# Kernel tuning notes

Measured on AMD Instinct MI355X. Metric: run time of the kernel, lower is better.

Reference implementation:

```python
import jax, jax.numpy as jnp
import numpy as np

D_MODEL = 1024
NUM_HEADS = 16
HEAD_DIM = D_MODEL // NUM_HEADS


def setup_inputs() -> dict:
    key = jax.random.key(0)
    ks = jax.random.split(key, 11)
    B, S, D = 2, 2048, D_MODEL
    scale = 1.0 / np.sqrt(D)
    inp = {
        "query": jax.random.normal(ks[0], (B, S, D), jnp.float32),
        "key": jax.random.normal(ks[1], (B, S, D), jnp.float32),
        "value": jax.random.normal(ks[2], (B, S, D), jnp.float32),
        "Wq": jax.random.normal(ks[3], (D, D), jnp.float32) * scale,
        "bq": jnp.zeros((D,), jnp.float32),
        "Wk": jax.random.normal(ks[4], (D, D), jnp.float32) * scale,
        "bk": jnp.zeros((D,), jnp.float32),
        "Wv": jax.random.normal(ks[5], (D, D), jnp.float32) * scale,
        "bv": jnp.zeros((D,), jnp.float32),
        "Wo": jax.random.normal(ks[6], (D, D), jnp.float32) * scale,
        "bo": jnp.zeros((D,), jnp.float32),
    }
    return inp


def reference(query, key, value, Wq, bq, Wk, bk, Wv, bv, Wo, bo):
    B, S, D = query.shape
    H, hd = NUM_HEADS, HEAD_DIM
    # linear projections (x @ W^T + b, torch nn.Linear convention)
    Q = query @ Wq.T + bq
    K = key @ Wk.T + bk
    V = value @ Wv.T + bv
    # split heads: [B, S, H, hd] -> [B, H, S, hd]
    Q = Q.reshape(B, S, H, hd).transpose(0, 2, 1, 3)
    K = K.reshape(B, S, H, hd).transpose(0, 2, 1, 3)
    V = V.reshape(B, S, H, hd).transpose(0, 2, 1, 3)
    # scaled dot-product attention (explicit, non-flash)
    scores = jnp.einsum("bhqd,bhkd->bhqk", Q, K) / jnp.sqrt(jnp.float32(hd)).astype(Q.dtype)
    attn = jax.nn.softmax(scores, axis=-1)
    out = jnp.einsum("bhqk,bhkd->bhqd", attn, V)
    # merge heads: [B, H, S, hd] -> [B, S, D]
    out = out.transpose(0, 2, 1, 3).reshape(B, S, D)
    return out @ Wo.T + bo
```

## Files before the change

### kernel.cpp

```cpp
#include <hip/hip_runtime.h>
#include <hip/hip_bf16.h>


constexpr int D_MODEL = 1024;
constexpr int S_LEN   = 2048;
constexpr int BATCH   = 2;
constexpr int NH      = 16;
constexpr int HD      = 64;
constexpr int ROWS    = BATCH * S_LEN;

typedef __attribute__((ext_vector_type(8))) short short8;
typedef __attribute__((ext_vector_type(4))) float float4a;

static __device__ __forceinline__ unsigned short f2bf(float f) {
  union { float f; unsigned u; } v{f};
  unsigned r = v.u + 0x7FFFu + ((v.u >> 16) & 1u);
  return (unsigned short)(r >> 16);
}

static __device__ __forceinline__ void async16(const void* g, void* l) {
  __builtin_amdgcn_global_load_lds(
      (const __attribute__((address_space(1))) unsigned int*)g,
      (__attribute__((address_space(3))) unsigned int*)l, 16, 0, 0);
}

struct ConvArgs { const float* s[7]; unsigned short* d[7]; int n[7]; };

__global__ __launch_bounds__(256) void convert_bf16(ConvArgs a) {
  const int which = blockIdx.y;
  const int i = (blockIdx.x * 256 + threadIdx.x) * 8;
  if (i >= a.n[which]) return;
  const float4* s = (const float4*)(a.s[which] + i);
  float4 x = s[0], y = s[1];
  unsigned short t[8] = {f2bf(x.x), f2bf(x.y), f2bf(x.z), f2bf(x.w),
                         f2bf(y.x), f2bf(y.y), f2bf(y.z), f2bf(y.w)};
  *(short8*)(a.d[which] + i) = *(short8*)t;
}

template <int MODE>
static __device__ __forceinline__ void gemm_body(const unsigned short* __restrict__ A,
                                                 const unsigned short* __restrict__ W,
                                                 const float* __restrict__ bias,
                                                 void* __restrict__ Yv, float scale) {
  __shared__ unsigned short As[128][32];
  __shared__ unsigned short Bs[128][32];
  const int tid = threadIdx.x;
  const int w = tid >> 6, lane = tid & 63;
  const int l15 = lane & 15, quad = lane >> 4;
  const int row0 = blockIdx.x * 128, col0 = blockIdx.y * 128;
  const int wm = (w & 1) * 64, wn = (w >> 1) * 64;

  const int srow = (w * 128 + lane) >> 2;
  const int schk = lane & 3;
  const unsigned short* Ap = A + (size_t)(row0 + srow) * D_MODEL + schk * 8;
  const unsigned short* Wp = W + (size_t)(col0 + srow) * D_MODEL + schk * 8;
  char* lA0 = (char*)As + w * 2048;
  char* lA1 = lA0 + 1024;
  char* lB0 = (char*)Bs + w * 2048;
  char* lB1 = lB0 + 1024;

  float4a acc[4][4];
#pragma unroll
  for (int i = 0; i < 4; i++)
#pragma unroll
    for (int j = 0; j < 4; j++) acc[i][j] = (float4a){0.f, 0.f, 0.f, 0.f};

  for (int kt = 0; kt < D_MODEL; kt += 32) {
    __syncthreads();
    async16(Ap + kt, lA0);
    async16(Ap + kt + 16 * D_MODEL, lA1);
    async16(Wp + kt, lB0);
    async16(Wp + kt + 16 * D_MODEL, lB1);
    __syncthreads();

    short8 af[4], bf[4];
#pragma unroll
    for (int mt = 0; mt < 4; mt++)
      af[mt] = *(const short8*)&As[wm + mt * 16 + l15][quad * 8];
#pragma unroll
    for (int nt = 0; nt < 4; nt++)
      bf[nt] = *(const short8*)&Bs[wn + nt * 16 + l15][quad * 8];
#pragma unroll
    for (int mt = 0; mt < 4; mt++)
#pragma unroll
      for (int nt = 0; nt < 4; nt++)
        acc[mt][nt] = __builtin_amdgcn_mfma_f32_16x16x32_bf16(af[mt], bf[nt], acc[mt][nt], 0, 0, 0);
  }

  int cols[4];
  float bvs[4];
#pragma unroll
  for (int nt = 0; nt < 4; nt++) {
    cols[nt] = col0 + wn + nt * 16 + l15;
    bvs[nt]  = bias[cols[nt]] * ((MODE == 0) ? scale : 1.0f);
  }

  if constexpr (MODE == 0) {
    unsigned short* Y = (unsigned short*)Yv;
#pragma unroll
    for (int mt = 0; mt < 4; mt++)
#pragma unroll
      for (int r = 0; r < 4; r++) {
        const int m = row0 + wm + mt * 16 + quad * 4 + r;
        const int bb = m >> 11, s = m & 2047;
#pragma unroll
        for (int nt = 0; nt < 4; nt++) {
          const int h = cols[nt] >> 6, d = cols[nt] & 63;
          Y[(((size_t)(bb * NH + h)) * S_LEN + s) * HD + d] =
              f2bf(acc[mt][nt][r] * scale + bvs[nt]);
        }
      }
  } else if constexpr (MODE == 2) {
    __shared__ unsigned short T[4][64][64];
#pragma unroll
    for (int mt = 0; mt < 4; mt++)
#pragma unroll
      for (int r = 0; r < 4; r++) {
        const int sl = mt * 16 + quad * 4 + r;
        const int cch = sl >> 3;
#pragma unroll
        for (int nt = 0; nt < 4; nt++) {
          const int dl = nt * 16 + l15;
          const int slot = cch ^ (dl & 7);
          T[w][dl][slot * 8 + (sl & 7)] = f2bf(acc[mt][nt][r] + bvs[nt]);
        }
      }
    asm volatile("s_waitcnt lgkmcnt(0)" ::: "memory");
    unsigned short* Y = (unsigned short*)Yv;
#pragma unroll
    for (int j = 0; j < 8; j++) {
      const int cid = j * 64 + lane;
      const int dl = cid >> 3;
      const int c  = cid & 7;
      const int slot = c ^ (dl & 7);
      short8 v = *(const short8*)&T[w][dl][slot * 8];
      const int col = col0 + wn + dl;
      const int h = col >> 6, d = col & 63;
      const int m = row0 + wm + c * 8;
      const int bb = m >> 11, s = m & 2047;
      *(short8*)&Y[(((size_t)(bb * NH + h)) * HD + d) * S_LEN + s] = v;
    }
  } else {
    float* Y = (float*)Yv;
#pragma unroll
    for (int mt = 0; mt < 4; mt++)
#pragma unroll
      for (int r = 0; r < 4; r++) {
        const int m = row0 + wm + mt * 16 + quad * 4 + r;
#pragma unroll
        for (int nt = 0; nt < 4; nt++)
          Y[(size_t)m * D_MODEL + cols[nt]] = acc[mt][nt][r] + bvs[nt];
      }
  }
}

__global__ __launch_bounds__(256) void gemm_qk(const unsigned short* q16, const unsigned short* k16,
                                               const unsigned short* wq, const unsigned short* wk,
                                               const float* bq, const float* bk,
                                               unsigned short* Q, unsigned short* K) {
  const bool z = (blockIdx.z != 0);
  gemm_body<0>(z ? k16 : q16, z ? wk : wq, z ? bk : bq, z ? (void*)K : (void*)Q,
               z ? 1.0f : 0.125f);
}

__global__ __launch_bounds__(256) void gemm_v(const unsigned short* v16, const unsigned short* wv,
                                              const float* bv, unsigned short* Vt) {
  gemm_body<2>(v16, wv, bv, Vt, 1.0f);
}

__global__ __launch_bounds__(256) void gemm_o(const unsigned short* o16, const unsigned short* wo,
                                              const float* bo, float* out) {
  gemm_body<3>(o16, wo, bo, out, 1.0f);
}

__global__ __launch_bounds__(256) void attn_kernel(
    const unsigned short* __restrict__ Qh, const unsigned short* __restrict__ Kh,
    const unsigned short* __restrict__ Vt, unsigned short* __restrict__ O) {
  const int qb = blockIdx.x;
  const int h  = blockIdx.y;
  const int bb = blockIdx.z;
  const int tid = threadIdx.x;
  const int w = tid >> 6, lane = tid & 63;
  const int l15 = lane & 15, quad = lane >> 4;

  __shared__ unsigned short Ks[64][72];
  __shared__ unsigned short Vs[64][72];
  __shared__ unsigned short Ps[4][32][72];

  const size_t bh = (size_t)(bb * NH + h);
  const unsigned short* Qp = Qh + bh * S_LEN * HD;
  const unsigned short* Kp = Kh + bh * S_LEN * HD;
  const unsigned short* Vp = Vt + bh * (size_t)HD * S_LEN;

  short8 qf[2][2];
#pragma unroll
  for (int qnt = 0; qnt < 2; qnt++)
#pragma unroll
    for (int c = 0; c < 2; c++)
      qf[qnt][c] = *(const short8*)(Qp + (size_t)(qb * 128 + w * 32 + qnt * 16 + l15) * HD +
                                    c * 32 + quad * 8);

  float4a Oacc[2][4];
#pragma unroll
  for (int a = 0; a < 2; a++)
#pragma unroll
    for (int b = 0; b < 4; b++) Oacc[a][b] = (float4a){0.f, 0.f, 0.f, 0.f};
  float lp[2] = {0.f, 0.f};

  for (int kb = 0; kb < S_LEN; kb += 64) {
    __syncthreads();
    {
      const unsigned short* src = Kp + (size_t)kb * HD;
#pragma unroll
      for (int r = 0; r < 2; r++) {
        const int idx = tid + r * 256;
        const int row = idx >> 3, cb = (idx & 7) * 8;
        *(short8*)&Ks[row][cb] = *(const short8*)(src + row * HD + cb);
      }
      const unsigned short* vsrc = Vp + kb;
#pragma unroll
      for (int r = 0; r < 2; r++) {
        const int idx = tid + r * 256;
        const int row = idx >> 3, cb = (idx & 7) * 8;
        *(short8*)&Vs[row][cb] = *(const short8*)(vsrc + (size_t)row * S_LEN + cb);
      }
    }
    __syncthreads();

#pragma unroll
    for (int mt = 0; mt < 4; mt++) {
      short8 a0 = *(const short8*)&Ks[mt * 16 + l15][quad * 8];
      short8 a1 = *(const short8*)&Ks[mt * 16 + l15][32 + quad * 8];
#pragma unroll
      for (int qnt = 0; qnt < 2; qnt++) {
        float4a s = (float4a){0.f, 0.f, 0.f, 0.f};
        s = __builtin_amdgcn_mfma_f32_16x16x32_bf16(a0, qf[qnt][0], s, 0, 0, 0);
        s = __builtin_amdgcn_mfma_f32_16x16x32_bf16(a1, qf[qnt][1], s, 0, 0, 0);
        const float p0 = __expf(s[0]), p1 = __expf(s[1]);
        const float p2 = __expf(s[2]), p3 = __expf(s[3]);
        lp[qnt] += (p0 + p1) + (p2 + p3);
        const unsigned u01 = (unsigned)f2bf(p0) | ((unsigned)f2bf(p1) << 16);
        const unsigned u23 = (unsigned)f2bf(p2) | ((unsigned)f2bf(p3) << 16);
        unsigned short* prow = &Ps[w][qnt * 16 + l15][mt * 16 + quad * 4];
        *(unsigned*)(prow)     = u01;
        *(unsigned*)(prow + 2) = u23;
      }
    }
    asm volatile("s_waitcnt lgkmcnt(0)" ::: "memory");

#pragma unroll
    for (int c = 0; c < 2; c++) {
      short8 pa0 = *(const short8*)&Ps[w][l15][c * 32 + quad * 8];
      short8 pa1 = *(const short8*)&Ps[w][16 + l15][c * 32 + quad * 8];
#pragma unroll
      for (int nt = 0; nt < 4; nt++) {
        short8 vb = *(const short8*)&Vs[nt * 16 + l15][c * 32 + quad * 8];
        Oacc[0][nt] = __builtin_amdgcn_mfma_f32_16x16x32_bf16(pa0, vb, Oacc[0][nt], 0, 0, 0);
        Oacc[1][nt] = __builtin_amdgcn_mfma_f32_16x16x32_bf16(pa1, vb, Oacc[1][nt], 0, 0, 0);
      }
    }
  }

#pragma unroll
  for (int qnt = 0; qnt < 2; qnt++) {
    lp[qnt] += __shfl_xor(lp[qnt], 16);
    lp[qnt] += __shfl_xor(lp[qnt], 32);
  }

#pragma unroll
  for (int qnt = 0; qnt < 2; qnt++) {
#pragma unroll
    for (int reg = 0; reg < 4; reg++) {
      const float lsum = __shfl(lp[qnt], quad * 4 + reg);
      const float rinv = 1.0f / lsum;
      const int q = qb * 128 + w * 32 + qnt * 16 + quad * 4 + reg;
      unsigned short* orow = O + ((size_t)bb * S_LEN + q) * D_MODEL + h * HD;
#pragma unroll
      for (int nt = 0; nt < 4; nt++)
        orow[nt * 16 + l15] = f2bf(Oacc[qnt][nt][reg] * rinv);
    }
  }
}

extern "C" void kernel_launch(void* const* d_in, const int* in_sizes, int n_in,
                              void* d_out, int out_size, void* d_ws, size_t ws_size,
                              hipStream_t stream) {
  const float* query = (const float*)d_in[0];
  const float* key   = (const float*)d_in[1];
  const float* value = (const float*)d_in[2];
  const float* Wq = (const float*)d_in[3];
  const float* bq = (const float*)d_in[4];
  const float* Wk = (const float*)d_in[5];
  const float* bk = (const float*)d_in[6];
  const float* Wv = (const float*)d_in[7];
  const float* bv = (const float*)d_in[8];
  const float* Wo = (const float*)d_in[9];
  const float* bo = (const float*)d_in[10];
  float* out = (float*)d_out;

  char* ws = (char*)d_ws;
  const size_t MB = 1024 * 1024;
  unsigned short* xq16 = (unsigned short*)(ws + 0 * MB);
  unsigned short* xk16 = (unsigned short*)(ws + 8 * MB);
  unsigned short* xv16 = (unsigned short*)(ws + 16 * MB);
  unsigned short* wq16 = (unsigned short*)(ws + 24 * MB);
  unsigned short* wk16 = (unsigned short*)(ws + 26 * MB);
  unsigned short* wv16 = (unsigned short*)(ws + 28 * MB);
  unsigned short* wo16 = (unsigned short*)(ws + 30 * MB);
  unsigned short* qbuf = (unsigned short*)(ws + 32 * MB);
  unsigned short* kbuf = (unsigned short*)(ws + 40 * MB);
  unsigned short* vtbuf = (unsigned short*)(ws + 48 * MB);
  unsigned short* obuf = (unsigned short*)(ws + 56 * MB);

  ConvArgs ca;
  const int NX = ROWS * D_MODEL, NW = D_MODEL * D_MODEL;
  ca.s[0] = query; ca.d[0] = xq16; ca.n[0] = NX;
  ca.s[1] = key;   ca.d[1] = xk16; ca.n[1] = NX;
  ca.s[2] = value; ca.d[2] = xv16; ca.n[2] = NX;
  ca.s[3] = Wq;    ca.d[3] = wq16; ca.n[3] = NW;
  ca.s[4] = Wk;    ca.d[4] = wk16; ca.n[4] = NW;
  ca.s[5] = Wv;    ca.d[5] = wv16; ca.n[5] = NW;
  ca.s[6] = Wo;    ca.d[6] = wo16; ca.n[6] = NW;
  hipLaunchKernelGGL(convert_bf16, dim3(NX / 2048, 7), dim3(256), 0, stream, ca);

  dim3 gqk(ROWS / 128, D_MODEL / 128, 2);
  hipLaunchKernelGGL(gemm_qk, gqk, dim3(256), 0, stream,
                     xq16, xk16, wq16, wk16, bq, bk, qbuf, kbuf);
  dim3 gg(ROWS / 128, D_MODEL / 128);
  hipLaunchKernelGGL(gemm_v, gg, dim3(256), 0, stream, xv16, wv16, bv, vtbuf);

  dim3 ga(S_LEN / 128, NH, BATCH);
  hipLaunchKernelGGL(attn_kernel, ga, dim3(256), 0, stream, qbuf, kbuf, vtbuf, obuf);

  hipLaunchKernelGGL(gemm_o, gg, dim3(256), 0, stream, obuf, wo16, bo, out);
}
```

Before: 273.1 us.

## Fuse QKV GEMMs, split attention over KV halves, swizzle LDS, retile output GEMM

Merges the Q/K and V projection launches into one three-slice grid, and rewrites GEMM and attention tile loads as swizzled async global-to-LDS copies to avoid bank conflicts. Attention is split into two KV halves per query block to double the grid, writing fp32 partial outputs and row sums that a new merge kernel combines and normalizes into bf16. The output GEMM uses 64-row tiles for more blocks. The split adds fp32 partial traffic and an extra launch in exchange for more parallelism.

```diff
diff --git a/kernel.cpp b/kernel.cpp
--- a/kernel.cpp
+++ b/kernel.cpp
@@ -37,60 +37,74 @@
   *(short8*)(a.d[which] + i) = *(short8*)t;
 }
 
-template <int MODE>
-static __device__ __forceinline__ void gemm_body(const unsigned short* __restrict__ A,
-                                                 const unsigned short* __restrict__ W,
-                                                 const float* __restrict__ bias,
-                                                 void* __restrict__ Yv, float scale) {
-  __shared__ unsigned short As[128][32];
-  __shared__ unsigned short Bs[128][32];
+template <int MODE, int BM>
+static __device__ __forceinline__ void gemm_body(
+    const unsigned short* __restrict__ A, const unsigned short* __restrict__ W,
+    const float* __restrict__ bias, void* __restrict__ Yv, float scale,
+    unsigned short* As, unsigned short* Bs, unsigned short* Tb) {
+  constexpr int NT = (BM == 128) ? 4 : 2;
   const int tid = threadIdx.x;
   const int w = tid >> 6, lane = tid & 63;
   const int l15 = lane & 15, quad = lane >> 4;
-  const int row0 = blockIdx.x * 128, col0 = blockIdx.y * 128;
-  const int wm = (w & 1) * 64, wn = (w >> 1) * 64;
-
-  const int srow = (w * 128 + lane) >> 2;
-  const int schk = lane & 3;
-  const unsigned short* Ap = A + (size_t)(row0 + srow) * D_MODEL + schk * 8;
-  const unsigned short* Wp = W + (size_t)(col0 + srow) * D_MODEL + schk * 8;
-  char* lA0 = (char*)As + w * 2048;
-  char* lA1 = lA0 + 1024;
-  char* lB0 = (char*)Bs + w * 2048;
-  char* lB1 = lB0 + 1024;
-
-  float4a acc[4][4];
+  const int row0 = blockIdx.x * BM, col0 = blockIdx.y * 128;
+  const int wm = (BM == 128) ? (w & 1) * 64 : 0;
+  const int wn = (BM == 128) ? (w >> 1) * 64 : w * 32;
+
+  float4a acc[4][NT];
 #pragma unroll
   for (int i = 0; i < 4; i++)
 #pragma unroll
-    for (int j = 0; j < 4; j++) acc[i][j] = (float4a){0.f, 0.f, 0.f, 0.f};
+    for (int j = 0; j < NT; j++) acc[i][j] = (float4a){0.f, 0.f, 0.f, 0.f};
+
+  const int swA = (quad + (wm >> 1) + (l15 >> 1)) & 3;
+  const int swB = (quad + (wn >> 1) + (l15 >> 1)) & 3;
 
   for (int kt = 0; kt < D_MODEL; kt += 32) {
     __syncthreads();
-    async16(Ap + kt, lA0);
-    async16(Ap + kt + 16 * D_MODEL, lA1);
-    async16(Wp + kt, lB0);
-    async16(Wp + kt + 16 * D_MODEL, lB1);
+#pragma unroll
+    for (int j = 0; j < 2; j++) {
+      const int i = w * 2 + j;
+      const int r = i * 16 + (lane >> 2);
+      const int c = ((lane & 3) - (r >> 1)) & 3;
+      async16(W + (size_t)(col0 + r) * D_MODEL + kt + c * 8, (char*)Bs + i * 1024);
+    }
+    if constexpr (BM == 128) {
+#pragma unroll
+      for (int j = 0; j < 2; j++) {
+        const int i = w * 2 + j;
+        const int r = i * 16 + (lane >> 2);
+        const int c = ((lane & 3) - (r >> 1)) & 3;
+        async16(A + (size_t)(row0 + r) * D_MODEL + kt + c * 8, (char*)As + i * 1024);
+      }
+    } else {
+      const int r = w * 16 + (lane >> 2);
+      const int c = ((lane & 3) - (r >> 1)) & 3;
+      async16(A + (size_t)(row0 + r) * D_MODEL + kt + c * 8, (char*)As + w * 1024);
+    }
     __syncthreads();
 
-    short8 af[4], bf[4];
+    short8 af[4], bf[NT];
+#pragma unroll
+    for (int mt = 0; mt < 4; mt++) {
+      const int r = wm + mt * 16 + l15;
+      af[mt] = *(const short8*)&As[(r * 4 + swA) * 8];
+    }
+#pragma unroll
+    for (int nt = 0; nt < NT; nt++) {
+      const int r = wn + nt * 16 + l15;
+      bf[nt] = *(const short8*)&Bs[(r * 4 + swB) * 8];
+    }
 #pragma unroll
     for (int mt = 0; mt < 4; mt++)
-      af[mt] = *(const short8*)&As[wm + mt * 16 + l15][quad * 8];
-#pragma unroll
-    for (int nt = 0; nt < 4; nt++)
-      bf[nt] = *(const short8*)&Bs[wn + nt * 16 + l15][quad * 8];
-#pragma unroll
-    for (int mt = 0; mt < 4; mt++)
-#pragma unroll
-      for (int nt = 0; nt < 4; nt++)
+#pragma unroll
+      for (int nt = 0; nt < NT; nt++)
         acc[mt][nt] = __builtin_amdgcn_mfma_f32_16x16x32_bf16(af[mt], bf[nt], acc[mt][nt], 0, 0, 0);
   }
 
-  int cols[4];
-  float bvs[4];
-#pragma unroll
-  for (int nt = 0; nt < 4; nt++) {
+  int cols[NT];
+  float bvs[NT];
+#pragma unroll
+  for (int nt = 0; nt < NT; nt++) {
     cols[nt] = col0 + wn + nt * 16 + l15;
     bvs[nt]  = bias[cols[nt]] * ((MODE == 0) ? scale : 1.0f);
   }
@@ -104,14 +118,14 @@
         const int m = row0 + wm + mt * 16 + quad * 4 + r;
         const int bb = m >> 11, s = m & 2047;
 #pragma unroll
-        for (int nt = 0; nt < 4; nt++) {
+        for (int nt = 0; nt < NT; nt++) {
           const int h = cols[nt] >> 6, d = cols[nt] & 63;
           Y[(((size_t)(bb * NH + h)) * S_LEN + s) * HD + d] =
               f2bf(acc[mt][nt][r] * scale + bvs[nt]);
         }
       }
   } else if constexpr (MODE == 2) {
-    __shared__ unsigned short T[4][64][64];
+    unsigned short* T = Tb + w * 64 * 64;
 #pragma unroll
     for (int mt = 0; mt < 4; mt++)
 #pragma unroll
@@ -119,10 +133,10 @@
         const int sl = mt * 16 + quad * 4 + r;
         const int cch = sl >> 3;
 #pragma unroll
-        for (int nt = 0; nt < 4; nt++) {
-          const int dl = nt * 16 + l15;
+        for (int nt = 0; nt < NT; nt++) {
+          const int dl = cols[nt] - col0 - wn;
           const int slot = cch ^ (dl & 7);
-          T[w][dl][slot * 8 + (sl & 7)] = f2bf(acc[mt][nt][r] + bvs[nt]);
+          T[dl * 64 + slot * 8 + (sl & 7)] = f2bf(acc[mt][nt][r] + bvs[nt]);
         }
       }
     asm volatile("s_waitcnt lgkmcnt(0)" ::: "memory");
@@ -133,7 +147,7 @@
       const int dl = cid >> 3;
       const int c  = cid & 7;
       const int slot = c ^ (dl & 7);
-      short8 v = *(const short8*)&T[w][dl][slot * 8];
+      short8 v = *(const short8*)&T[dl * 64 + slot * 8];
       const int col = col0 + wn + dl;
       const int h = col >> 6, d = col & 63;
       const int m = row0 + wm + c * 8;
@@ -148,43 +162,46 @@
       for (int r = 0; r < 4; r++) {
         const int m = row0 + wm + mt * 16 + quad * 4 + r;
 #pragma unroll
-        for (int nt = 0; nt < 4; nt++)
+        for (int nt = 0; nt < NT; nt++)
           Y[(size_t)m * D_MODEL + cols[nt]] = acc[mt][nt][r] + bvs[nt];
       }
   }
 }
 
-__global__ __launch_bounds__(256) void gemm_qk(const unsigned short* q16, const unsigned short* k16,
-                                               const unsigned short* wq, const unsigned short* wk,
-                                               const float* bq, const float* bk,
-                                               unsigned short* Q, unsigned short* K) {
-  const bool z = (blockIdx.z != 0);
-  gemm_body<0>(z ? k16 : q16, z ? wk : wq, z ? bk : bq, z ? (void*)K : (void*)Q,
-               z ? 1.0f : 0.125f);
-}
-
-__global__ __launch_bounds__(256) void gemm_v(const unsigned short* v16, const unsigned short* wv,
-                                              const float* bv, unsigned short* Vt) {
-  gemm_body<2>(v16, wv, bv, Vt, 1.0f);
+__global__ __launch_bounds__(256) void gemm_qkv(
+    const unsigned short* xq, const unsigned short* xk, const unsigned short* xv,
+    const unsigned short* wq, const unsigned short* wk, const unsigned short* wv,
+    const float* bq, const float* bk, const float* bv,
+    unsigned short* Q, unsigned short* K, unsigned short* Vt) {
+  __shared__ unsigned short As[128 * 32];
+  __shared__ unsigned short Bs[128 * 32];
+  __shared__ unsigned short Tb[4 * 64 * 64];
+  const int z = blockIdx.z;
+  if (z == 0)      gemm_body<0, 128>(xq, wq, bq, Q,  0.125f, As, Bs, Tb);
+  else if (z == 1) gemm_body<0, 128>(xk, wk, bk, K,  1.0f,   As, Bs, Tb);
+  else             gemm_body<2, 128>(xv, wv, bv, Vt, 1.0f,   As, Bs, Tb);
 }
 
 __global__ __launch_bounds__(256) void gemm_o(const unsigned short* o16, const unsigned short* wo,
                                               const float* bo, float* out) {
-  gemm_body<3>(o16, wo, bo, out, 1.0f);
+  __shared__ unsigned short As[64 * 32];
+  __shared__ unsigned short Bs[128 * 32];
+  gemm_body<3, 64>(o16, wo, bo, out, 1.0f, As, Bs, nullptr);
 }
 
 __global__ __launch_bounds__(256) void attn_kernel(
     const unsigned short* __restrict__ Qh, const unsigned short* __restrict__ Kh,
-    const unsigned short* __restrict__ Vt, unsigned short* __restrict__ O) {
+    const unsigned short* __restrict__ Vt, float* __restrict__ Op,
+    float* __restrict__ Lp) {
   const int qb = blockIdx.x;
   const int h  = blockIdx.y;
-  const int bb = blockIdx.z;
+  const int bb = blockIdx.z >> 1, sp = blockIdx.z & 1;
   const int tid = threadIdx.x;
   const int w = tid >> 6, lane = tid & 63;
   const int l15 = lane & 15, quad = lane >> 4;
 
-  __shared__ unsigned short Ks[64][72];
-  __shared__ unsigned short Vs[64][72];
+  __shared__ unsigned short Ks[64 * 64];
+  __shared__ unsigned short Vs[64 * 64];
   __shared__ unsigned short Ps[4][32][72];
 
   const size_t bh = (size_t)(bb * NH + h);
@@ -207,30 +224,26 @@
     for (int b = 0; b < 4; b++) Oacc[a][b] = (float4a){0.f, 0.f, 0.f, 0.f};
   float lp[2] = {0.f, 0.f};
 
-  for (int kb = 0; kb < S_LEN; kb += 64) {
+  const int sw0 = (quad + l15) & 7;
+  const int sw1 = (quad + 4 + l15) & 7;
+
+  for (int kb = sp * 1024; kb < sp * 1024 + 1024; kb += 64) {
     __syncthreads();
-    {
-      const unsigned short* src = Kp + (size_t)kb * HD;
-#pragma unroll
-      for (int r = 0; r < 2; r++) {
-        const int idx = tid + r * 256;
-        const int row = idx >> 3, cb = (idx & 7) * 8;
-        *(short8*)&Ks[row][cb] = *(const short8*)(src + row * HD + cb);
-      }
-      const unsigned short* vsrc = Vp + kb;
-#pragma unroll
-      for (int r = 0; r < 2; r++) {
-        const int idx = tid + r * 256;
-        const int row = idx >> 3, cb = (idx & 7) * 8;
-        *(short8*)&Vs[row][cb] = *(const short8*)(vsrc + (size_t)row * S_LEN + cb);
-      }
+#pragma unroll
+    for (int j = 0; j < 2; j++) {
+      const int i = w * 2 + j;
+      const int r = i * 8 + (lane >> 3);
+      const int c = ((lane & 7) - r) & 7;
+      async16(Kp + (size_t)(kb + r) * HD + c * 8, (char*)Ks + i * 1024);
+      async16(Vp + (size_t)r * S_LEN + kb + c * 8, (char*)Vs + i * 1024);
     }
     __syncthreads();
 
 #pragma unroll
     for (int mt = 0; mt < 4; mt++) {
-      short8 a0 = *(const short8*)&Ks[mt * 16 + l15][quad * 8];
-      short8 a1 = *(const short8*)&Ks[mt * 16 + l15][32 + quad * 8];
+      const int rb = (mt * 16 + l15) * 8;
+      short8 a0 = *(const short8*)&Ks[(rb + sw0) * 8];
+      short8 a1 = *(const short8*)&Ks[(rb + sw1) * 8];
 #pragma unroll
       for (int qnt = 0; qnt < 2; qnt++) {
         float4a s = (float4a){0.f, 0.f, 0.f, 0.f};
@@ -239,11 +252,10 @@
         const float p0 = __expf(s[0]), p1 = __expf(s[1]);
         const float p2 = __expf(s[2]), p3 = __expf(s[3]);
         lp[qnt] += (p0 + p1) + (p2 + p3);
-        const unsigned u01 = (unsigned)f2bf(p0) | ((unsigned)f2bf(p1) << 16);
-        const unsigned u23 = (unsigned)f2bf(p2) | ((unsigned)f2bf(p3) << 16);
-        unsigned short* prow = &Ps[w][qnt * 16 + l15][mt * 16 + quad * 4];
-        *(unsigned*)(prow)     = u01;
-        *(unsigned*)(prow + 2) = u23;
+        uint2 pk;
+        pk.x = (unsigned)f2bf(p0) | ((unsigned)f2bf(p1) << 16);
+        pk.y = (unsigned)f2bf(p2) | ((unsigned)f2bf(p3) << 16);
+        *(uint2*)&Ps[w][qnt * 16 + l15][mt * 16 + quad * 4] = pk;
       }
     }
     asm volatile("s_waitcnt lgkmcnt(0)" ::: "memory");
@@ -252,9 +264,10 @@
     for (int c = 0; c < 2; c++) {
       short8 pa0 = *(const short8*)&Ps[w][l15][c * 32 + quad * 8];
       short8 pa1 = *(const short8*)&Ps[w][16 + l15][c * 32 + quad * 8];
+      const int vsw = (c * 4 + quad + l15) & 7;
 #pragma unroll
       for (int nt = 0; nt < 4; nt++) {
-        short8 vb = *(const short8*)&Vs[nt * 16 + l15][c * 32 + quad * 8];
+        short8 vb = *(const short8*)&Vs[((nt * 16 + l15) * 8 + vsw) * 8];
         Oacc[0][nt] = __builtin_amdgcn_mfma_f32_16x16x32_bf16(pa0, vb, Oacc[0][nt], 0, 0, 0);
         Oacc[1][nt] = __builtin_amdgcn_mfma_f32_16x16x32_bf16(pa1, vb, Oacc[1][nt], 0, 0, 0);
       }
@@ -266,20 +279,44 @@
     lp[qnt] += __shfl_xor(lp[qnt], 16);
     lp[qnt] += __shfl_xor(lp[qnt], 32);
   }
-
+  if (quad == 0) {
+#pragma unroll
+    for (int qnt = 0; qnt < 2; qnt++) {
+      const int q = qb * 128 + w * 32 + qnt * 16 + l15;
+      Lp[(size_t)sp * ROWS * NH + ((size_t)bb * S_LEN + q) * NH + h] = lp[qnt];
+    }
+  }
+
+  float* Ob = Op + (size_t)sp * ROWS * D_MODEL;
 #pragma unroll
   for (int qnt = 0; qnt < 2; qnt++) {
 #pragma unroll
     for (int reg = 0; reg < 4; reg++) {
-      const float lsum = __shfl(lp[qnt], quad * 4 + reg);
-      const float rinv = 1.0f / lsum;
       const int q = qb * 128 + w * 32 + qnt * 16 + quad * 4 + reg;
-      unsigned short* orow = O + ((size_t)bb * S_LEN + q) * D_MODEL + h * HD;
+      float* orow = Ob + ((size_t)bb * S_LEN + q) * D_MODEL + h * HD;
 #pragma unroll
       for (int nt = 0; nt < 4; nt++)
-        orow[nt * 16 + l15] = f2bf(Oacc[qnt][nt][reg] * rinv);
-    }
-  }
+        orow[nt * 16 + l15] = Oacc[qnt][nt][reg];
+    }
+  }
+}
+
+__global__ __launch_bounds__(256) void merge_kernel(const float* __restrict__ Op,
+                                                    const float* __restrict__ Lp,
+                                                    unsigned short* __restrict__ obuf) {
+  const int e = (blockIdx.x * 256 + threadIdx.x) * 8;
+  const int row = e >> 10, h = (e & 1023) >> 6;
+  const float l = Lp[(size_t)row * NH + h] + Lp[(size_t)ROWS * NH + (size_t)row * NH + h];
+  const float rinv = 1.0f / l;
+  const float4* p0 = (const float4*)(Op + e);
+  const float4* p1 = (const float4*)(Op + (size_t)ROWS * D_MODEL + e);
+  float4 a = p0[0], b = p0[1], c = p1[0], d = p1[1];
+  unsigned short t[8] = {
+      f2bf((a.x + c.x) * rinv), f2bf((a.y + c.y) * rinv),
+      f2bf((a.z + c.z) * rinv), f2bf((a.w + c.w) * rinv),
+      f2bf((b.x + d.x) * rinv), f2bf((b.y + d.y) * rinv),
+      f2bf((b.z + d.z) * rinv), f2bf((b.w + d.w) * rinv)};
+  *(short8*)(obuf + e) = *(short8*)t;
 }
 
 extern "C" void kernel_launch(void* const* d_in, const int* in_sizes, int n_in,
@@ -306,11 +343,13 @@
   unsigned short* wq16 = (unsigned short*)(ws + 24 * MB);
   unsigned short* wk16 = (unsigned short*)(ws + 26 * MB);
   unsigned short* wv16 = (unsigned short*)(ws + 28 * MB);
-  unsigned short* wo16 = (unsigned short*)(ws + 30 * MB);
-  unsigned short* qbuf = (unsigned short*)(ws + 32 * MB);
-  unsigned short* kbuf = (unsigned short*)(ws + 40 * MB);
+  unsigned short* qbuf  = (unsigned short*)(ws + 32 * MB);
+  unsigned short* kbuf  = (unsigned short*)(ws + 40 * MB);
   unsigned short* vtbuf = (unsigned short*)(ws + 48 * MB);
-  unsigned short* obuf = (unsigned short*)(ws + 56 * MB);
+  unsigned short* wo16  = (unsigned short*)(ws + 56 * MB);
+  float* Lp  = (float*)(ws + 58 * MB);
+  float* Op  = (float*)(ws + 0 * MB);
+  unsigned short* obuf = qbuf;
 
   ConvArgs ca;
   const int NX = ROWS * D_MODEL, NW = D_MODEL * D_MODEL;
@@ -323,14 +362,17 @@
   ca.s[6] = Wo;    ca.d[6] = wo16; ca.n[6] = NW;
   hipLaunchKernelGGL(convert_bf16, dim3(NX / 2048, 7), dim3(256), 0, stream, ca);
 
-  dim3 gqk(ROWS / 128, D_MODEL / 128, 2);
-  hipLaunchKernelGGL(gemm_qk, gqk, dim3(256), 0, stream,
-                     xq16, xk16, wq16, wk16, bq, bk, qbuf, kbuf);
-  dim3 gg(ROWS / 128, D_MODEL / 128);
-  hipLaunchKernelGGL(gemm_v, gg, dim3(256), 0, stream, xv16, wv16, bv, vtbuf);
-
-  dim3 ga(S_LEN / 128, NH, BATCH);
-  hipLaunchKernelGGL(attn_kernel, ga, dim3(256), 0, stream, qbuf, kbuf, vtbuf, obuf);
-
-  hipLaunchKernelGGL(gemm_o, gg, dim3(256), 0, stream, obuf, wo16, bo, out);
-}
+  dim3 gqkv(ROWS / 128, D_MODEL / 128, 3);
+  hipLaunchKernelGGL(gemm_qkv, gqkv, dim3(256), 0, stream,
+                     xq16, xk16, xv16, wq16, wk16, wv16, bq, bk, bv,
+                     qbuf, kbuf, vtbuf);
+
+  dim3 ga(S_LEN / 128, NH, BATCH * 2);
+  hipLaunchKernelGGL(attn_kernel, ga, dim3(256), 0, stream, qbuf, kbuf, vtbuf, Op, Lp);
+
+  hipLaunchKernelGGL(merge_kernel, dim3(ROWS * D_MODEL / 2048), dim3(256), 0, stream,
+                     Op, Lp, obuf);
+
+  dim3 go(ROWS / 64, D_MODEL / 128);
+  hipLaunchKernelGGL(gemm_o, go, dim3(256), 0, stream, obuf, wo16, bo, out);
+}
```

New measurement: 243.1 us. -11.0%, faster.
